# Kernel optimization log

Hardware: AMD Instinct MI355X
Metric: run time of the kernel (lower is better)

## Reference

```python
import jax, jax.numpy as jnp
import numpy as np

DEPTH, E, H, S, V, B = 6, 1024, 16, 2048, 32000, 2
HD = E // H
EPS = 1e-5


def _layernorm(x, w, b):
    mu = jnp.mean(x, axis=-1, keepdims=True)
    var = jnp.mean(jnp.square(x - mu), axis=-1, keepdims=True)
    return (x - mu) * jax.lax.rsqrt(var + EPS) * w + b


def setup_inputs() -> dict:
    key = jax.random.key(0)
    ks = jax.random.split(key, 8)
    std = 0.02
    return {
        "idx": jax.random.randint(ks[0], (B, S), 0, V),
        "tok_emb": jax.random.normal(ks[1], (V, E), jnp.float32) * std,
        "pos_emb": jax.random.normal(ks[2], (S, E), jnp.float32) * std,
        "qkv_w": jax.random.normal(ks[3], (DEPTH, 3 * E, E), jnp.float32) * std,
        "qkv_b": jnp.zeros((DEPTH, 3 * E), jnp.float32),
        "ln1_w": jnp.ones((DEPTH, E), jnp.float32),
        "ln1_b": jnp.zeros((DEPTH, E), jnp.float32),
        "ln2_w": jnp.ones((DEPTH, E), jnp.float32),
        "ln2_b": jnp.zeros((DEPTH, E), jnp.float32),
        "ff1_w": jax.random.normal(ks[4], (DEPTH, 4 * E, E), jnp.float32) * std,
        "ff1_b": jnp.zeros((DEPTH, 4 * E), jnp.float32),
        "ff2_w": jax.random.normal(ks[5], (DEPTH, E, 4 * E), jnp.float32) * std,
        "ff2_b": jnp.zeros((DEPTH, E), jnp.float32),
        "fin_w": jnp.ones((E,), jnp.float32),
        "fin_b": jnp.zeros((E,), jnp.float32),
        "proj_w": jax.random.normal(ks[6], (V, E), jnp.float32) * std,
    }


def _block(x, qkv_w, qkv_b, ln1_w, ln1_b, ln2_w, ln2_b, ff1_w, ff1_b, ff2_w, ff2_b):
    bs, seq, _ = x.shape
    # --- causal MSA (dropout in eval mode -> identity) ---
    xn = _layernorm(x, ln1_w, ln1_b)
    qkv = xn @ qkv_w.T + qkv_b                      # [B,S,3E]
    qkv = qkv.reshape(bs, seq, 3, H, HD)
    q, k, v = (jnp.moveaxis(qkv[:, :, i], 1, 2) for i in range(3))  # [B,H,S,HD]
    scores = jnp.einsum("bhqd,bhkd->bhqk", q, k) / jnp.sqrt(jnp.float32(HD))
    causal = jnp.triu(jnp.ones((seq, seq), bool), k=1)
    scores = jnp.where(causal[None, None], -jnp.inf, scores)
    probs = jax.nn.softmax(scores, axis=-1)
    attn = jnp.einsum("bhqk,bhkd->bqhd", probs, v).reshape(bs, seq, E)
    x = x + attn
    # --- feedforward ---
    xn = _layernorm(x, ln2_w, ln2_b)
    h = jax.nn.gelu(xn @ ff1_w.T + ff1_b, approximate=False)
    x = x + (h @ ff2_w.T + ff2_b)
    return x


def reference(idx, tok_emb, pos_emb, qkv_w, qkv_b, ln1_w, ln1_b, ln2_w, ln2_b,
              ff1_w, ff1_b, ff2_w, ff2_b, fin_w, fin_b, proj_w):
    bs, seq = idx.shape
    x = tok_emb[idx] + pos_emb[jnp.arange(seq)][None]  # [B,S,E]
    for l in range(DEPTH):
        x = _block(x, qkv_w[l], qkv_b[l], ln1_w[l], ln1_b[l], ln2_w[l], ln2_b[l],
                   ff1_w[l], ff1_b[l], ff2_w[l], ff2_b[l])
    x = _layernorm(x, fin_w, fin_b)
    logits = x @ proj_w.T  # [B,S,V], final_proj has no bias
    return logits
```

## Files before the change

kernel.cpp:

```cpp
#include <hip/hip_runtime.h>
#include <hip/hip_bf16.h>

#define DEPTH 6
#define E 1024
#define H 16
#define S 2048
#define V 32000
#define BB 2
#define HD 64
#define NTOK (BB * S)

typedef __attribute__((ext_vector_type(8))) short bf16x8;
typedef __attribute__((ext_vector_type(4))) float f32x4;
typedef unsigned short us;

__device__ inline us f2bf(float f) {
    union { float f; unsigned u; } v; v.f = f;
    unsigned r = v.u + 0x7fff + ((v.u >> 16) & 1);
    return (us)(r >> 16);
}
__device__ inline float bf2f(us b) {
    union { unsigned u; float f; } v; v.u = ((unsigned)b) << 16;
    return v.f;
}

__device__ __forceinline__ void gld16(const us* g, us* l) {
    __builtin_amdgcn_global_load_lds(
        (const __attribute__((address_space(1))) unsigned int*)g,
        (__attribute__((address_space(3))) unsigned int*)l, 16, 0, 0);
}

__global__ __launch_bounds__(256) void cast_kernel(const float* __restrict__ in,
                                                   us* __restrict__ out, int n8) {
    int i = blockIdx.x * 256 + threadIdx.x;
    if (i >= n8) return;
    f32x4 a = __builtin_nontemporal_load((const f32x4*)in + 2 * (size_t)i);
    f32x4 b = __builtin_nontemporal_load((const f32x4*)in + 2 * (size_t)i + 1);
    uint4 o;
    o.x = f2bf(a[0]) | ((unsigned)f2bf(a[1]) << 16);
    o.y = f2bf(a[2]) | ((unsigned)f2bf(a[3]) << 16);
    o.z = f2bf(b[0]) | ((unsigned)f2bf(b[1]) << 16);
    o.w = f2bf(b[2]) | ((unsigned)f2bf(b[3]) << 16);
    ((uint4*)out)[i] = o;
}

__global__ __launch_bounds__(256) void embed_ln(const int* __restrict__ idx,
                                                const float* __restrict__ tok,
                                                const float* __restrict__ pos,
                                                const float* __restrict__ w,
                                                const float* __restrict__ b,
                                                float* __restrict__ x,
                                                us* __restrict__ out) {
    int t = blockIdx.x;
    int s = t & (S - 1);
    int tokid = idx[t];
    int tid = threadIdx.x;
    int c = tid * 4;
    float4 a = *(const float4*)&tok[(size_t)tokid * E + c];
    float4 p = *(const float4*)&pos[(size_t)s * E + c];
    float4 v; v.x = a.x + p.x; v.y = a.y + p.y; v.z = a.z + p.z; v.w = a.w + p.w;
    *(float4*)&x[(size_t)t * E + c] = v;

    float sum = v.x + v.y + v.z + v.w;
    float sq  = v.x * v.x + v.y * v.y + v.z * v.z + v.w * v.w;
    __shared__ float red[8];
    for (int o = 32; o > 0; o >>= 1) { sum += __shfl_xor(sum, o); sq += __shfl_xor(sq, o); }
    int wave = tid >> 6, lane = tid & 63;
    if (lane == 0) { red[wave] = sum; red[4 + wave] = sq; }
    __syncthreads();
    if (tid == 0) {
        red[0] = red[0] + red[1] + red[2] + red[3];
        red[4] = red[4] + red[5] + red[6] + red[7];
    }
    __syncthreads();
    float mean = red[0] * (1.0f / E);
    float var  = red[4] * (1.0f / E) - mean * mean;
    float rstd = rsqrtf(var + 1e-5f);
    float4 wv = *(const float4*)&w[c];
    float4 bv = *(const float4*)&b[c];
    unsigned a0 = f2bf((v.x - mean) * rstd * wv.x + bv.x);
    unsigned a1 = f2bf((v.y - mean) * rstd * wv.y + bv.y);
    unsigned a2 = f2bf((v.z - mean) * rstd * wv.z + bv.z);
    unsigned a3 = f2bf((v.w - mean) * rstd * wv.w + bv.w);
    uint2 o; o.x = a0 | (a1 << 16); o.y = a2 | (a3 << 16);
    *(uint2*)&out[(size_t)t * E + c] = o;
}

__global__ __launch_bounds__(256) void ln_kernel(const float* __restrict__ x,
                                                 const float* __restrict__ w,
                                                 const float* __restrict__ b,
                                                 us* __restrict__ out) {
    int row = blockIdx.x;
    int tid = threadIdx.x;
    int c = tid * 4;
    float4 v = *(const float4*)&x[(size_t)row * E + c];
    float s  = v.x + v.y + v.z + v.w;
    float sq = v.x * v.x + v.y * v.y + v.z * v.z + v.w * v.w;
    __shared__ float red[8];
    for (int o = 32; o > 0; o >>= 1) { s += __shfl_xor(s, o); sq += __shfl_xor(sq, o); }
    int wave = tid >> 6, lane = tid & 63;
    if (lane == 0) { red[wave] = s; red[4 + wave] = sq; }
    __syncthreads();
    if (tid == 0) {
        red[0] = red[0] + red[1] + red[2] + red[3];
        red[4] = red[4] + red[5] + red[6] + red[7];
    }
    __syncthreads();
    float mean = red[0] * (1.0f / E);
    float var  = red[4] * (1.0f / E) - mean * mean;
    float rstd = rsqrtf(var + 1e-5f);
    float4 wv = *(const float4*)&w[c];
    float4 bv = *(const float4*)&b[c];
    unsigned a0 = f2bf((v.x - mean) * rstd * wv.x + bv.x);
    unsigned a1 = f2bf((v.y - mean) * rstd * wv.y + bv.y);
    unsigned a2 = f2bf((v.z - mean) * rstd * wv.z + bv.z);
    unsigned a3 = f2bf((v.w - mean) * rstd * wv.w + bv.w);
    uint2 o; o.x = a0 | (a1 << 16); o.y = a2 | (a3 << 16);
    *(uint2*)&out[(size_t)row * E + c] = o;
}

__global__ __launch_bounds__(256) void combine_ln(const us* __restrict__ p012,
                                                  const us* __restrict__ p3,
                                                  const float* __restrict__ bias,
                                                  float* __restrict__ x,
                                                  const float* __restrict__ w,
                                                  const float* __restrict__ b,
                                                  us* __restrict__ out) {
    int row = blockIdx.x;
    int tid = threadIdx.x;
    int c = tid * 4;
    size_t base = (size_t)row * E + c;
    const size_t stride = (size_t)NTOK * E;
    float4 v = *(const float4*)&x[base];
    uint2 a0 = *(const uint2*)&p012[base];
    uint2 a1 = *(const uint2*)&p012[base + stride];
    uint2 a2 = *(const uint2*)&p012[base + 2 * stride];
    uint2 a3 = *(const uint2*)&p3[base];
    float4 bi = *(const float4*)&bias[c];
    v.x += bf2f((us)(a0.x & 0xffff)) + bf2f((us)(a1.x & 0xffff)) + bf2f((us)(a2.x & 0xffff)) + bf2f((us)(a3.x & 0xffff)) + bi.x;
    v.y += bf2f((us)(a0.x >> 16))    + bf2f((us)(a1.x >> 16))    + bf2f((us)(a2.x >> 16))    + bf2f((us)(a3.x >> 16))    + bi.y;
    v.z += bf2f((us)(a0.y & 0xffff)) + bf2f((us)(a1.y & 0xffff)) + bf2f((us)(a2.y & 0xffff)) + bf2f((us)(a3.y & 0xffff)) + bi.z;
    v.w += bf2f((us)(a0.y >> 16))    + bf2f((us)(a1.y >> 16))    + bf2f((us)(a2.y >> 16))    + bf2f((us)(a3.y >> 16))    + bi.w;
    *(float4*)&x[base] = v;

    float s  = v.x + v.y + v.z + v.w;
    float sq = v.x * v.x + v.y * v.y + v.z * v.z + v.w * v.w;
    __shared__ float red[8];
    for (int o = 32; o > 0; o >>= 1) { s += __shfl_xor(s, o); sq += __shfl_xor(sq, o); }
    int wave = tid >> 6, lane = tid & 63;
    if (lane == 0) { red[wave] = s; red[4 + wave] = sq; }
    __syncthreads();
    if (tid == 0) {
        red[0] = red[0] + red[1] + red[2] + red[3];
        red[4] = red[4] + red[5] + red[6] + red[7];
    }
    __syncthreads();
    float mean = red[0] * (1.0f / E);
    float var  = red[4] * (1.0f / E) - mean * mean;
    float rstd = rsqrtf(var + 1e-5f);
    float4 wv = *(const float4*)&w[c];
    float4 bv = *(const float4*)&b[c];
    unsigned b0 = f2bf((v.x - mean) * rstd * wv.x + bv.x);
    unsigned b1 = f2bf((v.y - mean) * rstd * wv.y + bv.y);
    unsigned b2 = f2bf((v.z - mean) * rstd * wv.z + bv.z);
    unsigned b3 = f2bf((v.w - mean) * rstd * wv.w + bv.w);
    uint2 o; o.x = b0 | (b1 << 16); o.y = b2 | (b3 << 16);
    *(uint2*)&out[base] = o;
}

#define GPH(dd, fb, STAGE, ISVM, IS12)                                              \
  {                                                                                 \
    bf16x8 afr0[2], afr1[2];                                                        \
    if ((fb) == 0) {                                                                \
      _Pragma("unroll")                                                             \
      for (int n = 0; n < 4; n++)                                                   \
        _Pragma("unroll")                                                           \
        for (int ks = 0; ks < 2; ks++)                                              \
          bfr[n][ks] = *(const bf16x8*)&lds[32768 + (dd) * 16384 +                  \
              (brow + n * 16) * 64 + ((ks * 4 + g4) ^ xg) * 8];                     \
    }                                                                               \
    _Pragma("unroll")                                                               \
    for (int ks = 0; ks < 2; ks++) {                                                \
      afr0[ks] = *(const bf16x8*)&lds[(dd) * 16384 + ((fb) >> 1) * 4096 +           \
          arow0 * 64 + ((ks * 4 + g4) ^ xg) * 8];                                   \
      afr1[ks] = *(const bf16x8*)&lds[(dd) * 16384 + ((fb) >> 1) * 4096 +           \
          arow1 * 64 + ((ks * 4 + g4) ^ xg) * 8];                                   \
    }                                                                               \
    STAGE;                                                                          \
    __builtin_amdgcn_sched_barrier(0);                                              \
    if (IS12) asm volatile("s_waitcnt lgkmcnt(8)" ::: "memory");                    \
    __builtin_amdgcn_s_barrier();                                                   \
    asm volatile("s_waitcnt lgkmcnt(0)" ::: "memory");                              \
    __builtin_amdgcn_sched_barrier(0);                                              \
    __builtin_amdgcn_s_setprio(1);                                                  \
    _Pragma("unroll")                                                               \
    for (int n = 0; n < 4; n++)                                                     \
      _Pragma("unroll")                                                             \
      for (int ks = 0; ks < 2; ks++) {                                              \
        acc[(fb)][n]     = __builtin_amdgcn_mfma_f32_16x16x32_bf16(afr0[ks], bfr[n][ks], acc[(fb)][n], 0, 0, 0);     \
        acc[(fb) + 1][n] = __builtin_amdgcn_mfma_f32_16x16x32_bf16(afr1[ks], bfr[n][ks], acc[(fb) + 1][n], 0, 0, 0); \
      }                                                                             \
    __builtin_amdgcn_s_setprio(0);                                                  \
    __builtin_amdgcn_sched_barrier(0);                                              \
    if ((ISVM) == 1) asm volatile("s_waitcnt vmcnt(6)" ::: "memory");               \
    if ((ISVM) == 2) asm volatile("s_waitcnt vmcnt(0)" ::: "memory");               \
    __builtin_amdgcn_s_barrier();                                                   \
  }

template <int OUT_BF16, int ACT_GELU, int HAS_BIAS, int SPLITK, int WRITE_VT>
__global__ __launch_bounds__(512, 2) void gemm256(const us* __restrict__ A, int lda,
                                                  const us* __restrict__ Bw, int ldb,
                                                  const float* __restrict__ bias,
                                                  void* __restrict__ outp,
                                                  void* __restrict__ outp3,
                                                  us* __restrict__ vt,
                                                  int M, int N, int K, int ldo) {
    __shared__ us lds[65536];
    int tid = threadIdx.x;
    int nwg = gridDim.x;
    int wgid = blockIdx.x;
    int chunk = nwg >> 3;
    int sw = (wgid & 7) * chunk + (wgid >> 3);
    int MB = M >> 8;
    int bm, bn;
    us* outb;
    float* outf = (float*)outp;
    if (SPLITK) {
        int ntile = MB * (N >> 8);
        int kz = sw / ntile;
        int rem = sw % ntile;
        bm = (rem % MB) * 256;
        bn = (rem / MB) * 256;
        A  += (size_t)kz * K;
        Bw += (size_t)kz * K;
        outb = (kz < 3) ? (us*)outp + (size_t)kz * M * ldo : (us*)outp3;
    } else {
        bm = (sw % MB) * 256;
        bn = (sw / MB) * 256;
        outb = (us*)outp;
    }
    int w = tid >> 6, lane = tid & 63;
    int wr = w >> 2, wc = w & 3;
    int l15 = lane & 15, g4 = lane >> 4;
    int xg = l15 & 7;
    int arow0 = (wr ? 32 : 0) + l15;
    int arow1 = arow0 + 16;
    int brow = wc * 64 + l15;
    int NT = K >> 6;

    f32x4 acc[8][4] = {};
    bf16x8 bfr[4][2];

    auto stA = [&](int u, int dd, int h) {
        #pragma unroll
        for (int i = 0; i < 2; i++) {
            int k = tid + i * 512;
            int q = 2 * h + (k >> 9);
            int r = (k >> 3) & 63;
            int tr = q * 32 + (r & 31) + ((r >> 5) << 7);
            int gp = (k & 7) ^ (r & 7);
            gld16(A + (size_t)(bm + tr) * lda + u * 64 + gp * 8,
                  &lds[dd * 16384 + h * 8192 + k * 8]);
        }
    };
    auto stB = [&](int u, int dd, int h) {
        #pragma unroll
        for (int i = 0; i < 2; i++) {
            int k = tid + i * 512;
            int row = h * 128 + (k >> 3);
            int gp = (k & 7) ^ ((k >> 3) & 7);
            gld16(Bw + (size_t)(bn + row) * ldb + u * 64 + gp * 8,
                  &lds[32768 + dd * 16384 + h * 8192 + k * 8]);
        }
    };

    stB(0, 0, 0); stB(0, 0, 1); stA(0, 0, 0); stA(0, 0, 1);
    stB(1, 1, 0); stB(1, 1, 1); stA(1, 1, 0);
    __builtin_amdgcn_sched_barrier(0);
    asm volatile("s_waitcnt vmcnt(6)" ::: "memory");
    __builtin_amdgcn_s_barrier();

    #pragma unroll 1
    for (int t = 0; t < NT - 2; t += 2) {
        GPH(0, 0, stA(t + 1, 1, 1), 0, 1)
        GPH(0, 2, stB(t + 2, 0, 0), 0, 0)
        GPH(0, 4, stB(t + 2, 0, 1), 0, 0)
        GPH(0, 6, stA(t + 2, 0, 0), 1, 0)
        GPH(1, 0, stA(t + 2, 0, 1), 0, 1)
        GPH(1, 2, stB(t + 3, 1, 0), 0, 0)
        GPH(1, 4, stB(t + 3, 1, 1), 0, 0)
        GPH(1, 6, stA(t + 3, 1, 0), 1, 0)
    }
    GPH(0, 0, stA(NT - 1, 1, 1), 0, 1)
    GPH(0, 2, , 0, 0)
    GPH(0, 4, , 0, 0)
    GPH(0, 6, , 2, 0)
    GPH(1, 0, , 0, 1)
    GPH(1, 2, , 0, 0)
    GPH(1, 4, , 0, 0)
    GPH(1, 6, , 0, 0)

    if (WRITE_VT && bn >= 2048) {
        #pragma unroll
        for (int mf = 0; mf < 8; mf++)
            #pragma unroll
            for (int n = 0; n < 4; n++) {
                int r = bm + wr * 128 + mf * 16 + g4 * 4;
                int c = bn + wc * 64 + n * 16 + l15;
                int hh = (c - 2048) >> 6, d = (c - 2048) & 63;
                int bq = r >> 11, s = r & (S - 1);
                float bv = HAS_BIAS ? bias[c] : 0.0f;
                unsigned o0 = f2bf(acc[mf][n][0] + bv) | ((unsigned)f2bf(acc[mf][n][1] + bv) << 16);
                unsigned o1 = f2bf(acc[mf][n][2] + bv) | ((unsigned)f2bf(acc[mf][n][3] + bv) << 16);
                uint2 pk; pk.x = o0; pk.y = o1;
                *(uint2*)&vt[(((size_t)(bq * H + hh) * 64 + d) << 11) + s] = pk;
            }
        return;
    }
    #pragma unroll
    for (int mf = 0; mf < 8; mf++)
        #pragma unroll
        for (int n = 0; n < 4; n++)
            #pragma unroll
            for (int j = 0; j < 4; j++) {
                int r = bm + wr * 128 + mf * 16 + g4 * 4 + j;
                int c = bn + wc * 64 + n * 16 + l15;
                float v = acc[mf][n][j];
                if (HAS_BIAS) v += bias[c];
                if (ACT_GELU) v = 0.5f * v * (1.0f + erff(v * 0.70710678118f));
                if (OUT_BF16) outb[(size_t)r * ldo + c] = f2bf(v);
                else __builtin_nontemporal_store(v, &outf[(size_t)r * ldo + c]);
            }
}

__global__ __launch_bounds__(512, 4) void attn_kernel(const us* __restrict__ qkv,
                                                      const us* __restrict__ vT,
                                                      float* __restrict__ x) {
    int qt = blockIdx.x, h = blockIdx.y, b = blockIdx.z;
    if (b == 1) qt = (S / 128 - 1) - qt;
    int tid = threadIdx.x;
    int w = tid >> 6, lane = tid & 63;
    int l15 = lane & 15, g4 = lane >> 4;
    int s0 = qt * 128;
    int qrow_base = s0 + w * 16;
    const size_t qbase = (size_t)b * S * 3072;
    const size_t vtbase = ((size_t)(b * H + h) * 64) * S;

    __shared__ us K_lds[2][64 * 64];
    __shared__ us VT_lds[2][64 * 64];
    __shared__ us P_lds[8][16 * 72];

    bf16x8 q[2];
    #pragma unroll
    for (int dc = 0; dc < 2; dc++) {
        q[dc] = *(const bf16x8*)&qkv[qbase + (size_t)(qrow_base + l15) * 3072 + h * 64 + dc * 32 + 8 * g4];
        us* qq = (us*)&q[dc];
        #pragma unroll
        for (int e = 0; e < 8; e++) qq[e] = f2bf(bf2f(qq[e]) * 0.125f);
    }

    f32x4 O[4] = {};
    float m_run[4], l_part[4];
    #pragma unroll
    for (int j = 0; j < 4; j++) { m_run[j] = -INFINITY; l_part[j] = 0.0f; }

    int lastt = 2 * qt + 1;
    {
        int p = tid, row = p >> 3, cc = p & 7;
        int scc = cc ^ (row & 7);
        gld16(&qkv[qbase + (size_t)(0 + row) * 3072 + 1024 + h * 64 + scc * 8], &K_lds[0][p * 8]);
        gld16(&vT[vtbase + (size_t)row * S + 0 + scc * 8], &VT_lds[0][p * 8]);
    }
    __syncthreads();

    for (int t = 0; t <= lastt; t++) {
        int bb = t & 1;
        if (t < lastt) {
            int p = tid, row = p >> 3, cc = p & 7;
            int scc = cc ^ (row & 7);
            gld16(&qkv[qbase + (size_t)((t + 1) * 64 + row) * 3072 + 1024 + h * 64 + scc * 8], &K_lds[bb ^ 1][p * 8]);
            gld16(&vT[vtbase + (size_t)row * S + (t + 1) * 64 + scc * 8], &VT_lds[bb ^ 1][p * 8]);
        }
        int k0 = t * 64;
        if (k0 <= qrow_base + 15) {
            f32x4 sf[4];
            __builtin_amdgcn_s_setprio(1);
            #pragma unroll
            for (int c = 0; c < 4; c++) {
                f32x4 z = {};
                int row = c * 16 + l15;
                #pragma unroll
                for (int dc = 0; dc < 2; dc++) {
                    int ch = (dc * 4 + g4) ^ (row & 7);
                    bf16x8 kb = *(const bf16x8*)&K_lds[bb][row * 64 + ch * 8];
                    z = __builtin_amdgcn_mfma_f32_16x16x32_bf16(q[dc], kb, z, 0, 0, 0);
                }
                sf[c] = z;
            }
            __builtin_amdgcn_s_setprio(0);
            bool needmask = (k0 + 63 > qrow_base);
            float vv[4][4], tmr[4];
            #pragma unroll
            for (int j = 0; j < 4; j++) {
                int qrow = qrow_base + g4 * 4 + j;
                float v0 = sf[0][j], v1 = sf[1][j];
                float v2 = sf[2][j], v3 = sf[3][j];
                if (needmask) {
                    if (k0 +      l15 > qrow) v0 = -INFINITY;
                    if (k0 + 16 + l15 > qrow) v1 = -INFINITY;
                    if (k0 + 32 + l15 > qrow) v2 = -INFINITY;
                    if (k0 + 48 + l15 > qrow) v3 = -INFINITY;
                }
                float tm = fmaxf(fmaxf(v0, v1), fmaxf(v2, v3));
                tm = fmaxf(tm, __shfl_xor(tm, 1, 16));
                tm = fmaxf(tm, __shfl_xor(tm, 2, 16));
                tm = fmaxf(tm, __shfl_xor(tm, 4, 16));
                tm = fmaxf(tm, __shfl_xor(tm, 8, 16));
                tmr[j] = tm;
                vv[0][j] = v0; vv[1][j] = v1; vv[2][j] = v2; vv[3][j] = v3;
            }
            bool grow = (tmr[0] > m_run[0] + 8.0f) || (tmr[1] > m_run[1] + 8.0f) ||
                        (tmr[2] > m_run[2] + 8.0f) || (tmr[3] > m_run[3] + 8.0f);
            bool skip = !__any(grow);
            float pr[4][4], alpha[4];
            #pragma unroll
            for (int j = 0; j < 4; j++) {
                float mnew = skip ? m_run[j] : fmaxf(m_run[j], tmr[j]);
                float p0 = __expf(vv[0][j] - mnew), p1 = __expf(vv[1][j] - mnew);
                float p2 = __expf(vv[2][j] - mnew), p3 = __expf(vv[3][j] - mnew);
                float sum4 = (p0 + p1) + (p2 + p3);
                if (skip) {
                    l_part[j] += sum4;
                } else {
                    alpha[j] = __expf(m_run[j] - mnew);
                    l_part[j] = l_part[j] * alpha[j] + sum4;
                    m_run[j] = mnew;
                }
                pr[0][j] = p0; pr[1][j] = p1; pr[2][j] = p2; pr[3][j] = p3;
            }
            if (!skip) {
                #pragma unroll
                for (int f = 0; f < 4; f++)
                    #pragma unroll
                    for (int j = 0; j < 4; j++) O[f][j] *= alpha[j];
            }
            us* Pw = &P_lds[w][0];
            #pragma unroll
            for (int c = 0; c < 4; c++)
                #pragma unroll
                for (int j = 0; j < 4; j++)
                    Pw[(g4 * 4 + j) * 72 + c * 16 + l15] = f2bf(pr[c][j]);
            __builtin_amdgcn_s_setprio(1);
            #pragma unroll
            for (int kc = 0; kc < 2; kc++) {
                bf16x8 pa = *(const bf16x8*)&Pw[l15 * 72 + kc * 32 + g4 * 8];
                #pragma unroll
                for (int dt = 0; dt < 4; dt++) {
                    int row = dt * 16 + l15;
                    int ch = (kc * 4 + g4) ^ (row & 7);
                    bf16x8 vb = *(const bf16x8*)&VT_lds[bb][row * 64 + ch * 8];
                    O[dt] = __builtin_amdgcn_mfma_f32_16x16x32_bf16(pa, vb, O[dt], 0, 0, 0);
                }
            }
            __builtin_amdgcn_s_setprio(0);
        }
        __syncthreads();
    }
    float l_run[4];
    #pragma unroll
    for (int j = 0; j < 4; j++) {
        float l = l_part[j];
        l += __shfl_xor(l, 1, 16);
        l += __shfl_xor(l, 2, 16);
        l += __shfl_xor(l, 4, 16);
        l += __shfl_xor(l, 8, 16);
        l_run[j] = l;
    }
    #pragma unroll
    for (int dt = 0; dt < 4; dt++)
        #pragma unroll
        for (int j = 0; j < 4; j++) {
            size_t o = ((size_t)b * S + qrow_base + g4 * 4 + j) * E + h * 64 + dt * 16 + l15;
            x[o] += O[dt][j] / l_run[j];
        }
}

extern "C" void kernel_launch(void* const* d_in, const int* in_sizes, int n_in,
                              void* d_out, int out_size, void* d_ws, size_t ws_size,
                              hipStream_t stream) {
    const int*   idx    = (const int*)d_in[0];
    const float* tok    = (const float*)d_in[1];
    const float* pos    = (const float*)d_in[2];
    const float* qkv_w  = (const float*)d_in[3];
    const float* qkv_b  = (const float*)d_in[4];
    const float* ln1_w  = (const float*)d_in[5];
    const float* ln1_b  = (const float*)d_in[6];
    const float* ln2_w  = (const float*)d_in[7];
    const float* ln2_b  = (const float*)d_in[8];
    const float* ff1_w  = (const float*)d_in[9];
    const float* ff1_b  = (const float*)d_in[10];
    const float* ff2_w  = (const float*)d_in[11];
    const float* ff2_b  = (const float*)d_in[12];
    const float* fin_w  = (const float*)d_in[13];
    const float* fin_b  = (const float*)d_in[14];
    const float* proj_w = (const float*)d_in[15];

    char* ws = (char*)d_ws;
    float* x    = (float*)ws;
    us*    xn   = (us*)(ws + 16777216);
    us*    qkvb = (us*)(ws + 25165824);
    us*    hbuf = (us*)(ws + 50331648);
    us*    wbuf = (us*)(ws + 83886080);
    us*    vTb  = (us*)(ws + 92274688);
    us*    pbuf = qkvb;

    embed_ln<<<NTOK, 256, 0, stream>>>(idx, tok, pos, ln1_w, ln1_b, x, xn);
    for (int l = 0; l < DEPTH; l++) {
        cast_kernel<<<1536, 256, 0, stream>>>(qkv_w + (size_t)l * 3 * E * E, wbuf, 3 * E * E / 8);
        gemm256<1, 0, 1, 0, 1><<<192, 512, 0, stream>>>(
            xn, E, wbuf, E, qkv_b + l * 3 * E, qkvb, nullptr, vTb, NTOK, 3 * E, E, 3 * E);
        attn_kernel<<<dim3(S / 128, H, BB), 512, 0, stream>>>(qkvb, vTb, x);
        ln_kernel<<<NTOK, 256, 0, stream>>>(x, ln2_w + l * E, ln2_b + l * E, xn);
        cast_kernel<<<2048, 256, 0, stream>>>(ff1_w + (size_t)l * 4 * E * E, wbuf, 4 * E * E / 8);
        gemm256<1, 1, 1, 0, 0><<<256, 512, 0, stream>>>(
            xn, E, wbuf, E, ff1_b + l * 4 * E, hbuf, nullptr, nullptr, NTOK, 4 * E, E, 4 * E);
        cast_kernel<<<2048, 256, 0, stream>>>(ff2_w + (size_t)l * E * 4 * E, wbuf, 4 * E * E / 8);
        gemm256<1, 0, 0, 1, 0><<<256, 512, 0, stream>>>(
            hbuf, 4 * E, wbuf, 4 * E, nullptr, qkvb, vTb, nullptr, NTOK, E, E, E);
        const float* nw = (l < DEPTH - 1) ? (ln1_w + (l + 1) * E) : fin_w;
        const float* nb = (l < DEPTH - 1) ? (ln1_b + (l + 1) * E) : fin_b;
        combine_ln<<<NTOK, 256, 0, stream>>>(qkvb, vTb, ff2_b + l * E, x, nw, nb, xn);
    }
    cast_kernel<<<16000, 256, 0, stream>>>(proj_w, pbuf, V * E / 8);
    gemm256<0, 0, 0, 0, 0><<<2000, 512, 0, stream>>>(
        xn, E, pbuf, E, nullptr, d_out, nullptr, nullptr, NTOK, V, E, V);
}
```

Measured before the change: 1.697 ms.

## Fold fp32-to-bf16 weight casts into extra workgroups of preceding GEMMs

Adds rider workgroups to the QKV and FF1 GEMM launches. They cast the next GEMM's fp32 weights (ff1, ff2) to bf16 while the matmul workgroups run. The ff1 weights are written into unused columns of the qkv buffer with a stride of 3072, so the cast kernels drop out and their work overlaps with GEMM compute. The risk is that rider blocks compete for bandwidth and CU slots, and the buffer aliasing depends on attention no longer needing those qkv columns.

```diff
diff --git a/kernel.cpp b/kernel.cpp
--- a/kernel.cpp
+++ b/kernel.cpp
@@ -207,19 +207,38 @@
     __builtin_amdgcn_s_barrier();                                                   \
   }
 
-template <int OUT_BF16, int ACT_GELU, int HAS_BIAS, int SPLITK, int WRITE_VT>
+template <int OUT_BF16, int ACT_GELU, int HAS_BIAS, int SPLITK, int WRITE_VT, int RIDER>
 __global__ __launch_bounds__(512, 2) void gemm256(const us* __restrict__ A, int lda,
                                                   const us* __restrict__ Bw, int ldb,
                                                   const float* __restrict__ bias,
                                                   void* __restrict__ outp,
                                                   void* __restrict__ outp3,
                                                   us* __restrict__ vt,
+                                                  const float* __restrict__ csrc,
+                                                  us* __restrict__ cdst,
+                                                  int dst_ld, int gemm_nwg,
                                                   int M, int N, int K, int ldo) {
+    int tid = threadIdx.x;
+    int wgid = blockIdx.x;
+    if (RIDER && wgid >= gemm_nwg) {
+        int nrb = gridDim.x - gemm_nwg;
+        int rtid = (wgid - gemm_nwg) * 512 + tid;
+        int nthr = nrb * 512;
+        for (int j = rtid; j < 4 * E * E / 8; j += nthr) {
+            f32x4 a = __builtin_nontemporal_load((const f32x4*)csrc + 2 * (size_t)j);
+            f32x4 b = __builtin_nontemporal_load((const f32x4*)csrc + 2 * (size_t)j + 1);
+            uint4 o;
+            o.x = f2bf(a[0]) | ((unsigned)f2bf(a[1]) << 16);
+            o.y = f2bf(a[2]) | ((unsigned)f2bf(a[3]) << 16);
+            o.z = f2bf(b[0]) | ((unsigned)f2bf(b[1]) << 16);
+            o.w = f2bf(b[2]) | ((unsigned)f2bf(b[3]) << 16);
+            int n = j >> 7, c8 = (j & 127) << 3;
+            *(uint4*)&cdst[(size_t)n * dst_ld + c8] = o;
+        }
+        return;
+    }
     __shared__ us lds[65536];
-    int tid = threadIdx.x;
-    int nwg = gridDim.x;
-    int wgid = blockIdx.x;
-    int chunk = nwg >> 3;
+    int chunk = gemm_nwg >> 3;
     int sw = (wgid & 7) * chunk + (wgid >> 3);
     int MB = M >> 8;
     int bm, bn;
@@ -517,21 +536,23 @@
     embed_ln<<<NTOK, 256, 0, stream>>>(idx, tok, pos, ln1_w, ln1_b, x, xn);
     for (int l = 0; l < DEPTH; l++) {
         cast_kernel<<<1536, 256, 0, stream>>>(qkv_w + (size_t)l * 3 * E * E, wbuf, 3 * E * E / 8);
-        gemm256<1, 0, 1, 0, 1><<<192, 512, 0, stream>>>(
-            xn, E, wbuf, E, qkv_b + l * 3 * E, qkvb, nullptr, vTb, NTOK, 3 * E, E, 3 * E);
+        gemm256<1, 0, 1, 0, 1, 1><<<256, 512, 0, stream>>>(
+            xn, E, wbuf, E, qkv_b + l * 3 * E, qkvb, nullptr, vTb,
+            ff1_w + (size_t)l * 4 * E * E, qkvb + 2048, 3072, 192, NTOK, 3 * E, E, 3 * E);
         attn_kernel<<<dim3(S / 128, H, BB), 512, 0, stream>>>(qkvb, vTb, x);
         ln_kernel<<<NTOK, 256, 0, stream>>>(x, ln2_w + l * E, ln2_b + l * E, xn);
-        cast_kernel<<<2048, 256, 0, stream>>>(ff1_w + (size_t)l * 4 * E * E, wbuf, 4 * E * E / 8);
-        gemm256<1, 1, 1, 0, 0><<<256, 512, 0, stream>>>(
-            xn, E, wbuf, E, ff1_b + l * 4 * E, hbuf, nullptr, nullptr, NTOK, 4 * E, E, 4 * E);
-        cast_kernel<<<2048, 256, 0, stream>>>(ff2_w + (size_t)l * E * 4 * E, wbuf, 4 * E * E / 8);
-        gemm256<1, 0, 0, 1, 0><<<256, 512, 0, stream>>>(
-            hbuf, 4 * E, wbuf, 4 * E, nullptr, qkvb, vTb, nullptr, NTOK, E, E, E);
+        gemm256<1, 1, 1, 0, 0, 1><<<320, 512, 0, stream>>>(
+            xn, E, qkvb + 2048, 3072, ff1_b + l * 4 * E, hbuf, nullptr, nullptr,
+            ff2_w + (size_t)l * E * 4 * E, wbuf, 1024, 256, NTOK, 4 * E, E, 4 * E);
+        gemm256<1, 0, 0, 1, 0, 0><<<256, 512, 0, stream>>>(
+            hbuf, 4 * E, wbuf, 4 * E, nullptr, qkvb, vTb, nullptr,
+            nullptr, nullptr, 0, 256, NTOK, E, E, E);
         const float* nw = (l < DEPTH - 1) ? (ln1_w + (l + 1) * E) : fin_w;
         const float* nb = (l < DEPTH - 1) ? (ln1_b + (l + 1) * E) : fin_b;
         combine_ln<<<NTOK, 256, 0, stream>>>(qkvb, vTb, ff2_b + l * E, x, nw, nb, xn);
     }
     cast_kernel<<<16000, 256, 0, stream>>>(proj_w, pbuf, V * E / 8);
-    gemm256<0, 0, 0, 0, 0><<<2000, 512, 0, stream>>>(
-        xn, E, pbuf, E, nullptr, d_out, nullptr, nullptr, NTOK, V, E, V);
-}
+    gemm256<0, 0, 0, 0, 0, 0><<<2000, 512, 0, stream>>>(
+        xn, E, pbuf, E, nullptr, d_out, nullptr, nullptr,
+        nullptr, nullptr, 0, 2000, NTOK, V, E, V);
+}
```

Measured after the change: 1.695 ms. About the same (-0.1%).
